# Performance work log

Hardware: AMD Instinct MI355X
Metric: run time of the kernel (lower is better)

Reference implementation:

```python
import jax, jax.numpy as jnp
import numpy as np

N_NODES = 50000
N_EDGES = 800000
F_IN = 1024
F_MID = 256
DROP_P = 0.5


def gcn_conv(x, W, b, src, dst, norm, n_nodes):
    # x: [N, Fin], W: [Fin, Fout]. PyG GCNConv: out = scatter(norm * (xW)[src] -> dst) + b
    h = x @ W                                  # [N, Fout]
    msg = h[src] * norm[:, None]               # [E+N, Fout] gathered, normalized messages
    out = jax.ops.segment_sum(msg, dst, num_segments=n_nodes)
    return out + b


def setup_inputs() -> dict:
    key = jax.random.key(0)
    k1, k2, k3, k4, k5 = jax.random.split(key, 5)
    x = jax.random.normal(k1, (N_NODES, F_IN), dtype=jnp.float32)
    edge_index = jax.random.randint(k2, (2, N_EDGES), 0, N_NODES, dtype=jnp.int64)
    # Glorot-ish init for GCN weights
    W1 = jax.random.normal(k3, (F_IN, F_MID), dtype=jnp.float32) / np.sqrt(F_IN)
    b1 = jnp.zeros((F_MID,), dtype=jnp.float32)
    W2 = jax.random.normal(k4, (F_MID, F_IN), dtype=jnp.float32) / np.sqrt(F_MID)
    b2 = jnp.zeros((F_IN,), dtype=jnp.float32)
    return {"x": x, "edge_index": edge_index, "W1": W1, "b1": b1, "W2": W2, "b2": b2}


def reference(x, edge_index, W1, b1, W2, b2):
    n = x.shape[0]
    # add self-loops (PyG GCNConv default add_self_loops=True)
    loop = jnp.arange(n, dtype=edge_index.dtype)
    src = jnp.concatenate([edge_index[0], loop])
    dst = jnp.concatenate([edge_index[1], loop])
    # symmetric normalization D^-1/2 (A+I) D^-1/2
    deg = jax.ops.segment_sum(jnp.ones_like(dst, dtype=x.dtype), dst, num_segments=n)
    dinv = jnp.where(deg > 0, jax.lax.rsqrt(deg), 0.0)
    norm = dinv[src] * dinv[dst]               # [E+N]

    h = jax.nn.relu(gcn_conv(x, W1, b1, src, dst, norm, n))
    # F.dropout(x) default: p=0.5, training=True -> deterministic mask w/ fixed key
    keep = jax.random.bernoulli(jax.random.key(42), 1.0 - DROP_P, h.shape)
    h = jnp.where(keep, h / (1.0 - DROP_P), 0.0)
    out = gcn_conv(h, W2, b2, src, dst, norm, n)
    return out
```

## Files before the change

kernel.cpp:

```cpp
#include <hip/hip_runtime.h>
#include <hip/hip_bf16.h>

#define N_NODES 50000
#define N_EDGES 800000
#define F_IN 1024
#define F_MID 256

typedef _Float16 f16;
typedef _Float16 f16x4 __attribute__((ext_vector_type(4)));
typedef _Float16 f16x8 __attribute__((ext_vector_type(8)));
typedef float f32x4 __attribute__((ext_vector_type(4)));

__device__ __forceinline__ void glds16(const f16* g, f16* l) {
    __builtin_amdgcn_global_load_lds(
        (const __attribute__((address_space(1))) unsigned int*)g,
        (__attribute__((address_space(3))) unsigned int*)l, 16, 0, 0);
}

__device__ __forceinline__ void tf_round(unsigned &x0, unsigned &x1, int r) {
    x0 += x1;
    x1 = (x1 << r) | (x1 >> (32 - r));
    x1 ^= x0;
}

__device__ __forceinline__ int keep_mask(unsigned f) {
    const unsigned ks0 = 0u, ks1 = 42u;
    const unsigned ks2 = ks0 ^ ks1 ^ 0x1BD11BDAu;
    unsigned x0 = 0u + ks0;
    unsigned x1 = f + ks1;
    tf_round(x0,x1,13); tf_round(x0,x1,15); tf_round(x0,x1,26); tf_round(x0,x1,6);
    x0 += ks1; x1 += ks2 + 1u;
    tf_round(x0,x1,17); tf_round(x0,x1,29); tf_round(x0,x1,16); tf_round(x0,x1,24);
    x0 += ks2; x1 += ks0 + 2u;
    tf_round(x0,x1,13); tf_round(x0,x1,15); tf_round(x0,x1,26); tf_round(x0,x1,6);
    x0 += ks0; x1 += ks1 + 3u;
    tf_round(x0,x1,17); tf_round(x0,x1,29); tf_round(x0,x1,16); tf_round(x0,x1,24);
    x0 += ks1; x1 += ks2 + 4u;
    tf_round(x0,x1,13); tf_round(x0,x1,15); tf_round(x0,x1,26); tf_round(x0,x1,6);
    x0 += ks2; x1 += ks0 + 5u;
    return (((x0 ^ x1) >> 31) == 0u);
}

__device__ __forceinline__ int ld_src(const int* ei, int e, int is64) {
    return is64 ? ei[2 * e] : ei[e];
}
__device__ __forceinline__ int ld_dst(const int* ei, int e, int is64) {
    return is64 ? ei[2 * N_EDGES + 2 * e] : ei[N_EDGES + e];
}

__global__ __launch_bounds__(256) void k_prep(const float* __restrict__ W1, f16* __restrict__ W1T,
                                              const int* __restrict__ ei,
                                              int* deg, int* cursor, int* counter, int* flag) {
    const int tid = threadIdx.x;
    const int gid = blockIdx.x * 256 + tid;
    const int gstr = gridDim.x * 256;
    if (gid < N_NODES) { deg[gid] = 0; cursor[gid] = 0; }
    if (gid == 0) counter[0] = 0;
    if (blockIdx.x == 0) {
        if (tid == 0) flag[0] = 1;
        __syncthreads();
        int nz = 0;
        for (int k = tid; k < 1024; k += 256) nz |= (ei[2 * k + 1] != 0);
        if (nz) atomicAnd(flag, 0);
    }
    for (int i = gid; i < F_IN * F_MID; i += gstr) {
        int k = i >> 8, n = i & 255;
        W1T[(size_t)n * F_IN + (k ^ ((n & 7) << 3))] = (f16)W1[i];
    }
}

__global__ __launch_bounds__(256) void k_rows(const int* __restrict__ deg, float* __restrict__ dinv,
                                              int* __restrict__ rowst, int* __restrict__ counter) {
    int i = blockIdx.x * 256 + threadIdx.x;
    if (i < N_NODES) {
        dinv[i] = rsqrtf((float)(deg[i] + 1));
        rowst[i] = atomicAdd(counter, deg[i]);
    }
}

__global__ __launch_bounds__(256) void k_fill(const int* __restrict__ ei, const int* __restrict__ rowst,
                                              int* __restrict__ cursor, int* __restrict__ csr,
                                              const int* __restrict__ flag) {
    int e = blockIdx.x * 256 + threadIdx.x;
    int is64 = flag[0];
    if (e < N_EDGES) {
        int d = ld_dst(ei, e, is64);
        int pos = rowst[d] + atomicAdd(&cursor[d], 1);
        csr[pos] = ld_src(ei, e, is64);
    }
}

template<int BM, int BN, int TN, bool A16, bool C16>
__global__ __launch_bounds__(TN) void k_mfma(const void* __restrict__ Ag,
                                             const f16* __restrict__ BTg,
                                             void* __restrict__ Cg,
                                             const float* __restrict__ bias,
                                             int M, int Ntot, int K, int mainx,
                                             const int* __restrict__ ei, int* __restrict__ deg,
                                             const int* __restrict__ flag,
                                             const float* __restrict__ Wr, f16* __restrict__ WrT) {
    if ((int)blockIdx.x >= mainx) {
        const int str = (gridDim.x - mainx) * TN;
        const int t0 = (blockIdx.x - mainx) * TN + threadIdx.x;
        const int is64 = flag[0];
        for (int e = t0; e < N_EDGES; e += str)
            atomicAdd(&deg[ld_dst(ei, e, is64)], 1);
        for (int i = t0; i < F_MID * F_IN; i += str) {
            int k = i >> 10, n = i & 1023;
            WrT[(size_t)n * F_MID + (k ^ ((n & 7) << 3))] = (f16)Wr[i];
        }
        return;
    }

    constexpr int BK = 64;
    constexpr int NW = TN / 64;
    constexpr int WM = BM / 64;
    constexpr int WN = NW / WM;
    constexpr int WTN = BN / WN;
    constexpr int FN = WTN / 16;
    constexpr int SMEM_STG = (2 * BM * BK + 2 * BN * BK) * 2;
    constexpr int LDC = BN + 8;
    constexpr int SMEM_EPI = BM * LDC * (C16 ? 2 : 4);
    constexpr int SMEM_SZ = SMEM_STG > SMEM_EPI ? SMEM_STG : SMEM_EPI;
    __shared__ __align__(16) char smem[SMEM_SZ];
    f16* As_ = (f16*)smem;
    f16* Bs_ = As_ + 2 * BM * BK;

    const int tid = threadIdx.x, lane = tid & 63, wid = tid >> 6;
    const int l15 = lane & 15;
    const int wm = wid % WM, wn = wid / WM;
    const int row0 = blockIdx.x * BM, col0 = blockIdx.y * BN;

    f32x4 acc[4][FN] = {};
    const int ar = tid >> 3;
    const int ac = (tid & 7) * 8;
    f32x4 av0 = {}, av1 = {};

    const int nkt = K / BK;
    int buf = 0;

    auto stage_load = [&](int kt, int b) {
        const int k0 = kt * BK;
        if constexpr (A16) {
            const f16* A = (const f16*)Ag;
            #pragma unroll
            for (int i = wid; i < BM * BK / 512; i += NW) {
                int li = i * 512 + lane * 8;
                int r = li >> 6, c = li & 63;
                glds16(&A[(size_t)(row0 + r) * K + k0 + c], &As_[b * BM * BK + i * 512]);
            }
        } else {
            const float* A = (const float*)Ag;
            int gr = row0 + ar;
            if (gr < M) {
                av0 = __builtin_nontemporal_load((const f32x4*)&A[(size_t)gr * K + k0 + ac]);
                av1 = __builtin_nontemporal_load((const f32x4*)&A[(size_t)gr * K + k0 + ac + 4]);
            } else { av0 = (f32x4){}; av1 = (f32x4){}; }
        }
        #pragma unroll
        for (int i = wid; i < BN * BK / 512; i += NW) {
            int li = i * 512 + lane * 8;
            int r = li >> 6, c = li & 63;
            glds16(&BTg[(size_t)(col0 + r) * K + k0 + c], &Bs_[b * BN * BK + i * 512]);
        }
    };
    auto stage_write = [&](int b) {
        if constexpr (!A16) {
            f16x4 l = __builtin_convertvector(av0, f16x4);
            f16x4 h = __builtin_convertvector(av1, f16x4);
            f16x8 v = { l[0], l[1], l[2], l[3], h[0], h[1], h[2], h[3] };
            *(f16x8*)&As_[b * BM * BK + ar * 64 + (ac ^ ((ar & 7) << 3))] = v;
        }
    };

    stage_load(0, 0);
    stage_write(0);
    __syncthreads();

    for (int kt = 0; kt < nkt; ++kt) {
        if (kt + 1 < nkt) stage_load(kt + 1, buf ^ 1);
        #pragma unroll
        for (int ks = 0; ks < 2; ++ks) {
            const int cc = ks * 32 + (lane >> 4) * 8;
            f16x8 af[4], bf[FN];
            #pragma unroll
            for (int m = 0; m < 4; ++m) {
                int r = wm * 64 + m * 16 + l15;
                af[m] = *(const f16x8*)&As_[buf * BM * BK + r * 64 + (cc ^ ((r & 7) << 3))];
            }
            #pragma unroll
            for (int n = 0; n < FN; ++n) {
                int r = wn * WTN + n * 16 + l15;
                bf[n] = *(const f16x8*)&Bs_[buf * BN * BK + r * 64 + (cc ^ ((r & 7) << 3))];
            }
            #pragma unroll
            for (int m = 0; m < 4; ++m)
                #pragma unroll
                for (int n = 0; n < FN; ++n)
                    acc[m][n] = __builtin_amdgcn_mfma_f32_16x16x32_f16(af[m], bf[n], acc[m][n], 0, 0, 0);
        }
        if (kt + 1 < nkt) stage_write(buf ^ 1);
        __syncthreads();
        buf ^= 1;
    }

    if constexpr (C16) {
        f16* CT = (f16*)smem;
        #pragma unroll
        for (int m = 0; m < 4; ++m)
            #pragma unroll
            for (int j = 0; j < 4; ++j) {
                const int rl = wm * 64 + m * 16 + (lane >> 4) * 4 + j;
                #pragma unroll
                for (int n = 0; n < FN; ++n)
                    CT[rl * LDC + wn * WTN + n * 16 + l15] = (f16)acc[m][n][j];
            }
        __syncthreads();
        f16* C = (f16*)Cg;
        constexpr int NCH = BM * BN / 8;
        #pragma unroll
        for (int ci = tid; ci < NCH; ci += TN) {
            const int r = ci / (BN / 8), c = (ci % (BN / 8)) * 8;
            const int gr = row0 + r;
            if (gr < M) {
                f16x8 v = *(const f16x8*)&CT[r * LDC + c];
                *(f16x8*)&C[(size_t)gr * Ntot + col0 + c] = v;
            }
        }
    } else {
        float* CT = (float*)smem;
        #pragma unroll
        for (int m = 0; m < 4; ++m)
            #pragma unroll
            for (int j = 0; j < 4; ++j) {
                const int rl = wm * 64 + m * 16 + (lane >> 4) * 4 + j;
                #pragma unroll
                for (int n = 0; n < FN; ++n)
                    CT[rl * LDC + wn * WTN + n * 16 + l15] = acc[m][n][j];
            }
        __syncthreads();
        float* C = (float*)Cg;
        constexpr int NCH = BM * BN / 4;
        #pragma unroll
        for (int ci = tid; ci < NCH; ci += TN) {
            const int r = ci / (BN / 4), c = (ci % (BN / 4)) * 4;
            const int gr = row0 + r;
            if (gr < M) {
                f32x4 v = *(const f32x4*)&CT[r * LDC + c];
                v += *(const f32x4*)&bias[col0 + c];
                __builtin_nontemporal_store(v, (f32x4*)&C[(size_t)gr * Ntot + col0 + c]);
            }
        }
    }
}

template<int POST, int SWZ, int SCALED_IN>
__global__ __launch_bounds__(256) void k_agg16(const f16* __restrict__ hin,
                                               f16* __restrict__ hout,
                                               const int* __restrict__ csr,
                                               const int* __restrict__ rowst,
                                               const int* __restrict__ deg,
                                               const float* __restrict__ dinv,
                                               const float* __restrict__ bias) {
    const int wid = threadIdx.x >> 6;
    const int lane = threadIdx.x & 63;
    const int row = blockIdx.x * 4 + wid;
    const int start = rowst[row];
    const int cnt = deg[row];
    const int ch = lane * 4;
    const float di = dinv[row];

    f32x4 acc = __builtin_convertvector(*(const f16x4*)&hin[(size_t)row * F_MID + ch], f32x4);
    if (!SCALED_IN) acc *= di;
    int k = 0;
    for (; k + 4 <= cnt; k += 4) {
        const int s0 = csr[start + k], s1 = csr[start + k + 1];
        const int s2 = csr[start + k + 2], s3 = csr[start + k + 3];
        f16x4 v0 = *(const f16x4*)&hin[(size_t)s0 * F_MID + ch];
        f16x4 v1 = *(const f16x4*)&hin[(size_t)s1 * F_MID + ch];
        f16x4 v2 = *(const f16x4*)&hin[(size_t)s2 * F_MID + ch];
        f16x4 v3 = *(const f16x4*)&hin[(size_t)s3 * F_MID + ch];
        if (SCALED_IN) {
            acc += __builtin_convertvector(v0, f32x4) + __builtin_convertvector(v1, f32x4)
                 + __builtin_convertvector(v2, f32x4) + __builtin_convertvector(v3, f32x4);
        } else {
            acc += dinv[s0] * __builtin_convertvector(v0, f32x4)
                 + dinv[s1] * __builtin_convertvector(v1, f32x4)
                 + dinv[s2] * __builtin_convertvector(v2, f32x4)
                 + dinv[s3] * __builtin_convertvector(v3, f32x4);
        }
    }
    for (; k < cnt; ++k) {
        const int s = csr[start + k];
        f32x4 v = __builtin_convertvector(*(const f16x4*)&hin[(size_t)s * F_MID + ch], f32x4);
        acc += SCALED_IN ? v : dinv[s] * v;
    }
    acc *= di;

    if (POST) {
        const unsigned f0 = (unsigned)row * F_MID + (unsigned)ch;
        #pragma unroll
        for (int j = 0; j < 4; ++j) {
            float t = acc[j] + bias[ch + j];
            t = fmaxf(t, 0.0f);
            t = keep_mask(f0 + j) ? t * 2.0f : 0.0f;
            acc[j] = t * di;
        }
    }
    const int oc = SWZ ? (ch ^ ((row & 7) << 3)) : ch;
    *(f16x4*)&hout[(size_t)row * F_MID + oc] = __builtin_convertvector(acc, f16x4);
}

extern "C" void kernel_launch(void* const* d_in, const int* in_sizes, int n_in,
                              void* d_out, int out_size, void* d_ws, size_t ws_size,
                              hipStream_t stream) {
    const float* x  = (const float*)d_in[0];
    const int*   ei = (const int*)d_in[1];
    const float* W1 = (const float*)d_in[2];
    const float* b1 = (const float*)d_in[3];
    const float* W2 = (const float*)d_in[4];
    const float* b2 = (const float*)d_in[5];
    float* out = (float*)d_out;

    f16* h0 = (f16*)out;
    f16* h1s = h0 + (size_t)N_NODES * F_MID;

    f16*   h2agg = (f16*)d_ws;
    f16*   W1T   = h2agg + (size_t)(N_NODES + 64) * F_MID;
    f16*   W2T   = W1T + (size_t)F_MID * F_IN;
    float* dinv  = (float*)(W2T + (size_t)F_IN * F_MID);
    int*   deg   = (int*)(dinv + N_NODES);
    int*   rowst = deg + N_NODES;
    int*   cursor= rowst + N_NODES;
    int*   csr   = cursor + N_NODES;
    int*   counter = csr + N_EDGES;
    int*   flag    = counter + 1;

    k_prep<<<256, 256, 0, stream>>>(W1, W1T, ei, deg, cursor, counter, flag);

    {
        const int mainx = (N_NODES + 63) / 64;
        dim3 grid(mainx + 240, 1);
        k_mfma<64, 256, 512, false, true><<<grid, 512, 0, stream>>>(
            (const void*)x, W1T, (void*)h0, nullptr, N_NODES, F_MID, F_IN,
            mainx, ei, deg, flag, W2, W2T);
    }

    k_rows<<<(N_NODES + 255) / 256, 256, 0, stream>>>(deg, dinv, rowst, counter);
    k_fill<<<(N_EDGES + 255) / 256, 256, 0, stream>>>(ei, rowst, cursor, csr, flag);

    k_agg16<1, 0, 0><<<N_NODES / 4, 256, 0, stream>>>(h0, h1s, csr, rowst, deg, dinv, b1);
    k_agg16<0, 1, 1><<<N_NODES / 4, 256, 0, stream>>>(h1s, h2agg, csr, rowst, deg, dinv, nullptr);

    {
        const int mainx = (N_NODES + 63) / 64;
        dim3 grid(mainx, 4);
        k_mfma<64, 256, 512, true, false><<<grid, 512, 0, stream>>>(
            (const void*)h2agg, W2T, (void*)out, b2, N_NODES, F_IN, F_MID,
            mainx, ei, deg, flag, W2, W2T);
    }
}
```

Before: 344.2 us.

## Add specialized first-layer GEMM with 16-row tiles and full-K fp16 A staging

Replaces the generic 64x256 MFMA kernel for the first layer (x @ W1) with a dedicated kernel that processes 16-row tiles. Each block converts its whole 16x1024 fp32 slice of x to fp16 into swizzled LDS once, using nontemporal loads, and double-buffers the W1T tiles through direct global-to-LDS loads. The aim is more blocks in flight and streaming of the large x read at full bandwidth. In exchange, W1T is re-read by many more blocks and the per-block MFMA work is smaller. The degree-count and W2 transpose side work still runs in the extra blocks.

```diff
diff --git a/kernel.cpp b/kernel.cpp
--- a/kernel.cpp
+++ b/kernel.cpp
@@ -87,6 +87,108 @@
         int d = ld_dst(ei, e, is64);
         int pos = rowst[d] + atomicAdd(&cursor[d], 1);
         csr[pos] = ld_src(ei, e, is64);
+    }
+}
+
+__global__ __launch_bounds__(512) void k_mfma1(const float* __restrict__ Ag,
+                                               const f16* __restrict__ BTg,
+                                               f16* __restrict__ Cg,
+                                               int mainx,
+                                               const int* __restrict__ ei, int* __restrict__ deg,
+                                               const int* __restrict__ flag,
+                                               const float* __restrict__ Wr, f16* __restrict__ WrT) {
+    constexpr int BM = 16, BN = 256, TN = 512, K = 1024, BK = 64;
+    constexpr int NW = 8, WTN = 32, FN = 2;
+
+    if ((int)blockIdx.x >= mainx) {
+        const int str = (gridDim.x - mainx) * TN;
+        const int t0 = (blockIdx.x - mainx) * TN + threadIdx.x;
+        const int is64 = flag[0];
+        for (int e = t0; e < N_EDGES; e += str)
+            atomicAdd(&deg[ld_dst(ei, e, is64)], 1);
+        for (int i = t0; i < F_MID * F_IN; i += str) {
+            int k = i >> 10, n = i & 1023;
+            WrT[(size_t)n * F_MID + (k ^ ((n & 7) << 3))] = (f16)Wr[i];
+        }
+        return;
+    }
+
+    __shared__ __align__(16) f16 As[BM * K];
+    __shared__ __align__(16) f16 Bs[2][BN * BK];
+
+    const int tid = threadIdx.x, lane = tid & 63, wid = tid >> 6;
+    const int l15 = lane & 15;
+    const int row0 = blockIdx.x * BM;
+
+    auto stage_load = [&](int kt, int b) {
+        const int k0 = kt * BK;
+        #pragma unroll
+        for (int i = wid; i < BN * BK / 512; i += NW) {
+            int li = i * 512 + lane * 8;
+            int r = li >> 6, c = li & 63;
+            glds16(&BTg[(size_t)r * K + k0 + c], &Bs[b][i * 512]);
+        }
+    };
+
+    stage_load(0, 0);
+
+    {
+        f32x4 lo[4], hi[4];
+        #pragma unroll
+        for (int p = 0; p < 4; ++p) {
+            int idx = p * TN + tid;
+            int r = idx >> 7, c8 = (idx & 127) * 8;
+            const float* src = &Ag[(size_t)(row0 + r) * K + c8];
+            lo[p] = __builtin_nontemporal_load((const f32x4*)src);
+            hi[p] = __builtin_nontemporal_load((const f32x4*)(src + 4));
+        }
+        #pragma unroll
+        for (int p = 0; p < 4; ++p) {
+            int idx = p * TN + tid;
+            int r = idx >> 7, c8 = (idx & 127) * 8;
+            f16x4 a = __builtin_convertvector(lo[p], f16x4);
+            f16x4 b = __builtin_convertvector(hi[p], f16x4);
+            f16x8 v = { a[0],a[1],a[2],a[3], b[0],b[1],b[2],b[3] };
+            *(f16x8*)&As[r * K + (c8 ^ ((r & 7) << 3))] = v;
+        }
+    }
+    __syncthreads();
+
+    f32x4 acc[FN] = {};
+    int buf = 0;
+    for (int kt = 0; kt < K / BK; ++kt) {
+        if (kt + 1 < K / BK) stage_load(kt + 1, buf ^ 1);
+        #pragma unroll
+        for (int ks = 0; ks < 2; ++ks) {
+            const int ccB = ks * 32 + (lane >> 4) * 8;
+            const int ccA = kt * BK + ccB;
+            f16x8 af = *(const f16x8*)&As[l15 * K + (ccA ^ ((l15 & 7) << 3))];
+            #pragma unroll
+            for (int n = 0; n < FN; ++n) {
+                int r = wid * WTN + n * 16 + l15;
+                f16x8 bf = *(const f16x8*)&Bs[buf][r * 64 + (ccB ^ ((r & 7) << 3))];
+                acc[n] = __builtin_amdgcn_mfma_f32_16x16x32_f16(af, bf, acc[n], 0, 0, 0);
+            }
+        }
+        __syncthreads();
+        buf ^= 1;
+    }
+
+    constexpr int LDC = BN + 8;
+    f16* CT = (f16*)Bs;
+    #pragma unroll
+    for (int j = 0; j < 4; ++j) {
+        const int rl = (lane >> 4) * 4 + j;
+        #pragma unroll
+        for (int n = 0; n < FN; ++n)
+            CT[rl * LDC + wid * WTN + n * 16 + l15] = (f16)acc[n][j];
+    }
+    __syncthreads();
+    {
+        const int ci = tid;
+        const int r = ci >> 5, c = (ci & 31) * 8;
+        f16x8 v = *(const f16x8*)&CT[r * LDC + c];
+        *(f16x8*)&Cg[(size_t)(row0 + r) * BN + c] = v;
     }
 }
 
@@ -339,11 +441,9 @@
     k_prep<<<256, 256, 0, stream>>>(W1, W1T, ei, deg, cursor, counter, flag);
 
     {
-        const int mainx = (N_NODES + 63) / 64;
+        const int mainx = N_NODES / 16;
         dim3 grid(mainx + 240, 1);
-        k_mfma<64, 256, 512, false, true><<<grid, 512, 0, stream>>>(
-            (const void*)x, W1T, (void*)h0, nullptr, N_NODES, F_MID, F_IN,
-            mainx, ei, deg, flag, W2, W2T);
+        k_mfma1<<<grid, 512, 0, stream>>>(x, W1T, h0, mainx, ei, deg, flag, W2, W2T);
     }
 
     k_rows<<<(N_NODES + 255) / 256, 256, 0, stream>>>(deg, dinv, rowst, counter);
```

Result: slower. 413.7 us (+20.2%).
